# Optimization experiments

Measured on AMD Instinct MI355X. Metric: run time of the kernel, lower is better.

The kernel has to match this reference:

```python
import jax, jax.numpy as jnp
import numpy as np

B, LQ, LK, D = 32, 2048, 2048, 64


def setup_inputs() -> dict:
    key = jax.random.key(0)
    k1, k2, k3, k4 = jax.random.split(key, 4)
    querys = jax.random.normal(k1, (B, LQ, D), dtype=jnp.float32)
    keys = jax.random.normal(k2, (B, LK, D), dtype=jnp.float32)
    values = jax.random.normal(k3, (B, LK, D), dtype=jnp.float32)
    # valid lengths in [1, LK]
    valid_lens = jax.random.randint(k4, (B,), 1, LK + 1, dtype=jnp.int32)
    return {"querys": querys, "keys": keys, "values": values, "valid_lens": valid_lens}


def reference(querys, keys, values, valid_lens):
    d = querys.shape[-1]
    # [B, Lq, Lk] score matrix
    scores = jnp.einsum("bqd,bkd->bqk", querys, keys) / jnp.sqrt(jnp.asarray(d, querys.dtype))
    # masked softmax: key positions >= valid_len get -1e6 (as in d2l masked_softmax)
    key_pos = jnp.arange(scores.shape[-1], dtype=jnp.int32)  # [Lk]
    mask = key_pos[None, None, :] < valid_lens[:, None, None]  # [B, 1, Lk]
    scores = jnp.where(mask, scores, jnp.asarray(-1e6, scores.dtype))
    attn = jax.nn.softmax(scores, axis=-1)
    # dropout p=0.0 -> identity
    return jnp.einsum("bqk,bkd->bqd", attn, values)
```

## Files before the change

### kernel.cpp

```cpp
#include <hip/hip_runtime.h>
#include <hip/hip_bf16.h>
#include <math.h>


#define B_    32
#define LQ_   2048
#define LK_   2048
#define D_    64

typedef __attribute__((ext_vector_type(8)))  short bf16x8;
typedef __attribute__((ext_vector_type(4)))  float f32x4;
typedef __attribute__((ext_vector_type(16))) float f32x16;

static __device__ __forceinline__ unsigned pk_bf16(float a, float b) {
    __hip_bfloat162 h = __float22bfloat162_rn(float2{a, b});
    return *(unsigned*)&h;
}

__global__ __launch_bounds__(128, 2) void fa_mfma3_kernel(
    const float* __restrict__ Q, const float* __restrict__ K,
    const float* __restrict__ V, const int* __restrict__ vlen,
    float* __restrict__ O)
{
    __shared__ __align__(16) short Kl[2][64 * 64];
    __shared__ __align__(16) short Vt[2][64 * 64];

    const int tid  = threadIdx.x;
    const int wave = tid >> 6;
    const int lane = tid & 63;
    const int c31  = lane & 31;
    const int h    = lane >> 5;

    const int b  = blockIdx.y;
    const int q0 = blockIdx.x * 64 + wave * 32;
    const int vl = vlen[b];
    const int nt = (vl + 63) >> 6;

    const float qscale = 0.125f * 1.44269504088896340736f;

    unsigned qfrag[4][4];
#pragma unroll
    for (int ks = 0; ks < 4; ++ks) {
        const float* qp = Q + ((size_t)(b * LQ_ + q0 + c31)) * D_ + ks * 16 + h * 8;
        f32x4 t0 = *(const f32x4*)qp;
        f32x4 t1 = *(const f32x4*)(qp + 4);
#pragma unroll
        for (int jj = 0; jj < 2; ++jj) {
            qfrag[ks][jj]     = pk_bf16(t0[2*jj] * qscale, t0[2*jj+1] * qscale);
            qfrag[ks][jj + 2] = pk_bf16(t1[2*jj] * qscale, t1[2*jj+1] * qscale);
        }
    }

    f32x16 oacc[2];
#pragma unroll
    for (int dt = 0; dt < 2; ++dt)
#pragma unroll
        for (int r = 0; r < 16; ++r) oacc[dt][r] = 0.f;
    float mrun = -INFINITY, lrun = 0.f;

    const int skey = tid >> 1, skh = tid & 1;
    const int vkg = tid >> 4, vdg = tid & 15;

    const float* kgp = K + ((size_t)(b * LK_ + skey)) * D_ + skh * 32;
    const float* vgp = V + ((size_t)(b * LK_ + vkg * 8)) * D_ + vdg * 4;

    f32x4 kr[8], vr[8];
#pragma unroll
    for (int i = 0; i < 8; ++i) kr[i] = *(const f32x4*)(kgp + 4 * i);
#pragma unroll
    for (int i = 0; i < 8; ++i) vr[i] = *(const f32x4*)(vgp + (size_t)i * D_);

    for (int t = 0; t < nt; ++t) {
        const int k0 = t * 64;
        const int buf = t & 1;

        {
            unsigned pk32[16];
#pragma unroll
            for (int m = 0; m < 16; ++m)
                pk32[m] = pk_bf16(kr[m >> 1][2 * (m & 1)], kr[m >> 1][2 * (m & 1) + 1]);
#pragma unroll
            for (int cch = 0; cch < 4; ++cch) {
                const int pos = (skh * 4 + cch) ^ (skey & 7);
                *(bf16x8*)&Kl[buf][skey * 64 + pos * 8] = *(bf16x8*)&pk32[4 * cch];
            }
#pragma unroll
            for (int dr = 0; dr < 4; ++dr) {
                unsigned w[4];
#pragma unroll
                for (int p = 0; p < 4; ++p)
                    w[p] = pk_bf16(vr[2 * p][dr], vr[2 * p + 1][dr]);
                const int dim = vdg * 4 + dr;
                const int pos = vkg ^ (dim & 7);
                *(bf16x8*)&Vt[buf][dim * 64 + pos * 8] = *(bf16x8*)&w[0];
            }
        }
        if (t + 1 < nt) {
            const float* kn = kgp + (size_t)(k0 + 64) * D_;
            const float* vn = vgp + (size_t)(k0 + 64) * D_;
#pragma unroll
            for (int i = 0; i < 8; ++i) kr[i] = *(const f32x4*)(kn + 4 * i);
#pragma unroll
            for (int i = 0; i < 8; ++i) vr[i] = *(const f32x4*)(vn + (size_t)i * D_);
        }
        __syncthreads();

        f32x16 st[2];
#pragma unroll
        for (int s = 0; s < 2; ++s) {
#pragma unroll
            for (int r = 0; r < 16; ++r) st[s][r] = 0.f;
#pragma unroll
            for (int ks = 0; ks < 4; ++ks) {
                const int pos = (ks * 2 + h) ^ (c31 & 7);
                bf16x8 kf = *(const bf16x8*)&Kl[buf][(s * 32 + c31) * 64 + pos * 8];
                st[s] = __builtin_amdgcn_mfma_f32_32x32x16_bf16(
                    kf, *(const bf16x8*)&qfrag[ks][0], st[s], 0, 0, 0);
            }
        }

        if (k0 + 64 > vl) {
#pragma unroll
            for (int s = 0; s < 2; ++s) {
                const int base = k0 + s * 32 + 4 * h;
#pragma unroll
                for (int r = 0; r < 16; ++r) {
                    const int key = base + (r & 3) + 8 * (r >> 2);
                    if (key >= vl) st[s][r] = -1e30f;
                }
            }
        }

        float tm = st[0][0];
#pragma unroll
        for (int s = 0; s < 2; ++s)
#pragma unroll
            for (int r = 0; r < 16; ++r) tm = fmaxf(tm, st[s][r]);
        tm = fmaxf(tm, __shfl_xor(tm, 32));
        const float mnew = fmaxf(mrun, tm);
        const float corr = exp2f(mrun - mnew);
        mrun = mnew;
        float rs = 0.f;
#pragma unroll
        for (int s = 0; s < 2; ++s)
#pragma unroll
            for (int r = 0; r < 16; ++r) {
                const float p = exp2f(st[s][r] - mnew);
                st[s][r] = p;
                rs += p;
            }
        rs += __shfl_xor(rs, 32);
        lrun = lrun * corr + rs;
#pragma unroll
        for (int dt = 0; dt < 2; ++dt)
#pragma unroll
            for (int r = 0; r < 16; ++r) oacc[dt][r] *= corr;

        unsigned pk[2][8];
#pragma unroll
        for (int s = 0; s < 2; ++s)
#pragma unroll
            for (int m = 0; m < 8; ++m)
                pk[s][m] = pk_bf16(st[s][2 * m], st[s][2 * m + 1]);

#pragma unroll
        for (int kq = 0; kq < 4; ++kq) {
            const int s = kq >> 1, A4 = (kq & 1) * 4;
            unsigned p0 = pk[s][A4], p1 = pk[s][A4+1], p2 = pk[s][A4+2], p3 = pk[s][A4+3];
            unsigned xp0 = __shfl_xor((int)p0, 32);
            unsigned xp1 = __shfl_xor((int)p1, 32);
            unsigned xp2 = __shfl_xor((int)p2, 32);
            unsigned xp3 = __shfl_xor((int)p3, 32);
            unsigned pf[4];
            pf[0] = h ? xp2 : p0;
            pf[1] = h ? xp3 : p1;
            pf[2] = h ? p2  : xp0;
            pf[3] = h ? p3  : xp1;
            const bf16x8 pfr = *(const bf16x8*)&pf[0];
#pragma unroll
            for (int dt = 0; dt < 2; ++dt) {
                const int pos = (kq * 2 + h) ^ (c31 & 7);
                bf16x8 vf = *(const bf16x8*)&Vt[buf][(dt * 32 + c31) * 64 + pos * 8];
                oacc[dt] = __builtin_amdgcn_mfma_f32_32x32x16_bf16(vf, pfr, oacc[dt], 0, 0, 0);
            }
        }
    }

    const float inv = 1.f / lrun;
    float* op = O + ((size_t)(b * LQ_ + q0 + c31)) * D_;
#pragma unroll
    for (int dt = 0; dt < 2; ++dt)
#pragma unroll
        for (int g = 0; g < 4; ++g) {
            f32x4 v;
#pragma unroll
            for (int j = 0; j < 4; ++j) v[j] = oacc[dt][4 * g + j] * inv;
            *(f32x4*)(op + dt * 32 + 8 * g + 4 * h) = v;
        }
}

extern "C" void kernel_launch(void* const* d_in, const int* in_sizes, int n_in,
                              void* d_out, int out_size, void* d_ws, size_t ws_size,
                              hipStream_t stream) {
    const float* Q    = (const float*)d_in[0];
    const float* K    = (const float*)d_in[1];
    const float* V    = (const float*)d_in[2];
    const int*   vlen = (const int*)d_in[3];
    float*       O    = (float*)d_out;

    dim3 grid(LQ_ / 64, B_);
    dim3 block(128);
    fa_mfma3_kernel<<<grid, block, 0, stream>>>(Q, K, V, vlen, O);
}
```

Baseline: 172.1 us.

## Split key dimension across chunks with a separate combine kernel

Adds a split-K (flash-decoding style) scheme in which each block handles one key chunk of up to four and writes unnormalized partial outputs plus running max and sum to workspace. A second kernel merges the chunks with log-sum-exp rescaling. The aim is to balance the load across batches with very different valid lengths and to fill the GPU with more blocks. In exchange it adds workspace traffic and an extra launch, and it drops K/V LDS double buffering so more blocks fit per CU. It also changes the V load mapping, uses the native exp2 builtin, and splits the max and sum reductions into parallel chains.

Result: slower. 305.3 us (+77.5%).

```diff
diff --git a/kernel.cpp b/kernel.cpp
--- a/kernel.cpp
+++ b/kernel.cpp
@@ -7,23 +7,31 @@
 #define LQ_   2048
 #define LK_   2048
 #define D_    64
+#define SLOTF (64 * 64 + 128)
 
 typedef __attribute__((ext_vector_type(8)))  short bf16x8;
 typedef __attribute__((ext_vector_type(4)))  float f32x4;
 typedef __attribute__((ext_vector_type(16))) float f32x16;
 
+#if defined(__has_builtin) && __has_builtin(__builtin_amdgcn_exp2f)
+#define EXP2(x) __builtin_amdgcn_exp2f(x)
+#else
+#define EXP2(x) exp2f(x)
+#endif
+
 static __device__ __forceinline__ unsigned pk_bf16(float a, float b) {
     __hip_bfloat162 h = __float22bfloat162_rn(float2{a, b});
     return *(unsigned*)&h;
 }
 
-__global__ __launch_bounds__(128, 2) void fa_mfma3_kernel(
+__global__ __launch_bounds__(128, 4) void fa_stage1(
     const float* __restrict__ Q, const float* __restrict__ K,
     const float* __restrict__ V, const int* __restrict__ vlen,
-    float* __restrict__ O)
+    float* __restrict__ O, float* __restrict__ ws,
+    int nchunks, int chunk_len, int direct)
 {
-    __shared__ __align__(16) short Kl[2][64 * 64];
-    __shared__ __align__(16) short Vt[2][64 * 64];
+    __shared__ __align__(16) short Kl[64 * 64];
+    __shared__ __align__(16) short Vt[64 * 64];
 
     const int tid  = threadIdx.x;
     const int wave = tid >> 6;
@@ -31,10 +39,13 @@
     const int c31  = lane & 31;
     const int h    = lane >> 5;
 
-    const int b  = blockIdx.y;
-    const int q0 = blockIdx.x * 64 + wave * 32;
+    const int qt = blockIdx.x, b = blockIdx.y, cidx = blockIdx.z;
     const int vl = vlen[b];
-    const int nt = (vl + 63) >> 6;
+    const int k_begin = cidx * chunk_len;
+    if (k_begin >= vl) return;
+    const int k_end = min(k_begin + chunk_len, vl);
+    const int nt = (k_end - k_begin + 63) >> 6;
+    const int q0 = qt * 64 + wave * 32;
 
     const float qscale = 0.125f * 1.44269504088896340736f;
 
@@ -59,10 +70,10 @@
     float mrun = -INFINITY, lrun = 0.f;
 
     const int skey = tid >> 1, skh = tid & 1;
-    const int vkg = tid >> 4, vdg = tid & 15;
-
-    const float* kgp = K + ((size_t)(b * LK_ + skey)) * D_ + skh * 32;
-    const float* vgp = V + ((size_t)(b * LK_ + vkg * 8)) * D_ + vdg * 4;
+    const int vkg  = tid & 7,  vdg = tid >> 3;
+
+    const float* kgp = K + ((size_t)(b * LK_ + k_begin + skey)) * D_ + skh * 32;
+    const float* vgp = V + ((size_t)(b * LK_ + k_begin + vkg * 8)) * D_ + vdg * 4;
 
     f32x4 kr[8], vr[8];
 #pragma unroll
@@ -71,8 +82,8 @@
     for (int i = 0; i < 8; ++i) vr[i] = *(const f32x4*)(vgp + (size_t)i * D_);
 
     for (int t = 0; t < nt; ++t) {
-        const int k0 = t * 64;
-        const int buf = t & 1;
+        const int k0 = k_begin + t * 64;
+        if (t) __syncthreads();
 
         {
             unsigned pk32[16];
@@ -82,7 +93,7 @@
 #pragma unroll
             for (int cch = 0; cch < 4; ++cch) {
                 const int pos = (skh * 4 + cch) ^ (skey & 7);
-                *(bf16x8*)&Kl[buf][skey * 64 + pos * 8] = *(bf16x8*)&pk32[4 * cch];
+                *(bf16x8*)&Kl[skey * 64 + pos * 8] = *(bf16x8*)&pk32[4 * cch];
             }
 #pragma unroll
             for (int dr = 0; dr < 4; ++dr) {
@@ -92,12 +103,12 @@
                     w[p] = pk_bf16(vr[2 * p][dr], vr[2 * p + 1][dr]);
                 const int dim = vdg * 4 + dr;
                 const int pos = vkg ^ (dim & 7);
-                *(bf16x8*)&Vt[buf][dim * 64 + pos * 8] = *(bf16x8*)&w[0];
+                *(bf16x8*)&Vt[dim * 64 + pos * 8] = *(bf16x8*)&w[0];
             }
         }
         if (t + 1 < nt) {
-            const float* kn = kgp + (size_t)(k0 + 64) * D_;
-            const float* vn = vgp + (size_t)(k0 + 64) * D_;
+            const float* kn = kgp + (size_t)(t + 1) * 64 * D_;
+            const float* vn = vgp + (size_t)(t + 1) * 64 * D_;
 #pragma unroll
             for (int i = 0; i < 8; ++i) kr[i] = *(const f32x4*)(kn + 4 * i);
 #pragma unroll
@@ -113,7 +124,7 @@
 #pragma unroll
             for (int ks = 0; ks < 4; ++ks) {
                 const int pos = (ks * 2 + h) ^ (c31 & 7);
-                bf16x8 kf = *(const bf16x8*)&Kl[buf][(s * 32 + c31) * 64 + pos * 8];
+                bf16x8 kf = *(const bf16x8*)&Kl[(s * 32 + c31) * 64 + pos * 8];
                 st[s] = __builtin_amdgcn_mfma_f32_32x32x16_bf16(
                     kf, *(const bf16x8*)&qfrag[ks][0], st[s], 0, 0, 0);
             }
@@ -131,24 +142,32 @@
             }
         }
 
-        float tm = st[0][0];
+        float mg[8];
 #pragma unroll
         for (int s = 0; s < 2; ++s)
 #pragma unroll
-            for (int r = 0; r < 16; ++r) tm = fmaxf(tm, st[s][r]);
+            for (int g = 0; g < 4; ++g)
+                mg[s * 4 + g] = fmaxf(fmaxf(st[s][4*g], st[s][4*g+1]),
+                                      fmaxf(st[s][4*g+2], st[s][4*g+3]));
+        float tm = fmaxf(fmaxf(fmaxf(mg[0], mg[1]), fmaxf(mg[2], mg[3])),
+                         fmaxf(fmaxf(mg[4], mg[5]), fmaxf(mg[6], mg[7])));
         tm = fmaxf(tm, __shfl_xor(tm, 32));
         const float mnew = fmaxf(mrun, tm);
-        const float corr = exp2f(mrun - mnew);
+        const float corr = EXP2(mrun - mnew);
         mrun = mnew;
-        float rs = 0.f;
+        float rs0 = 0.f, rs1 = 0.f, rs2 = 0.f, rs3 = 0.f;
 #pragma unroll
         for (int s = 0; s < 2; ++s)
 #pragma unroll
-            for (int r = 0; r < 16; ++r) {
-                const float p = exp2f(st[s][r] - mnew);
-                st[s][r] = p;
-                rs += p;
-            }
+            for (int g = 0; g < 4; ++g) {
+                float p0 = EXP2(st[s][4*g]   - mnew);
+                float p1 = EXP2(st[s][4*g+1] - mnew);
+                float p2 = EXP2(st[s][4*g+2] - mnew);
+                float p3 = EXP2(st[s][4*g+3] - mnew);
+                st[s][4*g] = p0; st[s][4*g+1] = p1; st[s][4*g+2] = p2; st[s][4*g+3] = p3;
+                rs0 += p0; rs1 += p1; rs2 += p2; rs3 += p3;
+            }
+        float rs = (rs0 + rs1) + (rs2 + rs3);
         rs += __shfl_xor(rs, 32);
         lrun = lrun * corr + rs;
 #pragma unroll
@@ -180,23 +199,72 @@
 #pragma unroll
             for (int dt = 0; dt < 2; ++dt) {
                 const int pos = (kq * 2 + h) ^ (c31 & 7);
-                bf16x8 vf = *(const bf16x8*)&Vt[buf][(dt * 32 + c31) * 64 + pos * 8];
+                bf16x8 vf = *(const bf16x8*)&Vt[(dt * 32 + c31) * 64 + pos * 8];
                 oacc[dt] = __builtin_amdgcn_mfma_f32_32x32x16_bf16(vf, pfr, oacc[dt], 0, 0, 0);
             }
         }
     }
 
-    const float inv = 1.f / lrun;
-    float* op = O + ((size_t)(b * LQ_ + q0 + c31)) * D_;
-#pragma unroll
-    for (int dt = 0; dt < 2; ++dt)
-#pragma unroll
-        for (int g = 0; g < 4; ++g) {
-            f32x4 v;
-#pragma unroll
-            for (int j = 0; j < 4; ++j) v[j] = oacc[dt][4 * g + j] * inv;
-            *(f32x4*)(op + dt * 32 + 8 * g + 4 * h) = v;
-        }
+    if (direct) {
+        const float inv = 1.f / lrun;
+        float* op = O + ((size_t)(b * LQ_ + q0 + c31)) * D_;
+#pragma unroll
+        for (int dt = 0; dt < 2; ++dt)
+#pragma unroll
+            for (int g = 0; g < 4; ++g) {
+                f32x4 v;
+#pragma unroll
+                for (int j = 0; j < 4; ++j) v[j] = oacc[dt][4 * g + j] * inv;
+                *(f32x4*)(op + dt * 32 + 8 * g + 4 * h) = v;
+            }
+    } else {
+        float* base = ws + (size_t)((b * 32 + qt) * nchunks + cidx) * SLOTF;
+        float* pp = base + (size_t)(wave * 32 + c31) * D_;
+#pragma unroll
+        for (int dt = 0; dt < 2; ++dt)
+#pragma unroll
+            for (int g = 0; g < 4; ++g) {
+                f32x4 v;
+#pragma unroll
+                for (int j = 0; j < 4; ++j) v[j] = oacc[dt][4 * g + j];
+                *(f32x4*)(pp + dt * 32 + 8 * g + 4 * h) = v;
+            }
+        if (h == 0) {
+            base[64 * 64 + wave * 32 + c31]      = mrun;
+            base[64 * 64 + 64 + wave * 32 + c31] = lrun;
+        }
+    }
+}
+
+__global__ __launch_bounds__(256) void fa_combine(
+    const float* __restrict__ ws, const int* __restrict__ vlen,
+    float* __restrict__ O, int nchunks, int chunk_len)
+{
+    const int idx = blockIdx.x * 256 + threadIdx.x;
+    const int b  = idx >> 15;
+    const int r  = idx & 32767;
+    const int q  = r >> 4;
+    const int dg = r & 15;
+    const int vl = vlen[b];
+    const int nc = min(nchunks, (vl + chunk_len - 1) / chunk_len);
+    const int qt = q >> 6, ql = q & 63;
+    const size_t sbase = (size_t)((b * 32 + qt) * nchunks) * SLOTF;
+
+    float M = -INFINITY;
+    for (int c = 0; c < nc; ++c)
+        M = fmaxf(M, ws[sbase + (size_t)c * SLOTF + 64 * 64 + ql]);
+
+    f32x4 acc = (f32x4){0.f, 0.f, 0.f, 0.f};
+    float L = 0.f;
+    for (int c = 0; c < nc; ++c) {
+        const float* sb = ws + sbase + (size_t)c * SLOTF;
+        const float w = EXP2(sb[64 * 64 + ql] - M);
+        L += sb[64 * 64 + 64 + ql] * w;
+        f32x4 o4 = *(const f32x4*)(sb + (size_t)ql * D_ + dg * 4);
+        acc += o4 * w;
+    }
+    const float inv = 1.f / L;
+    *(f32x4*)(O + (size_t)(b * LQ_ + q) * D_ + dg * 4) = acc * inv;
 }
 
 extern "C" void kernel_launch(void* const* d_in, const int* in_sizes, int n_in,
@@ -207,8 +275,17 @@
     const float* V    = (const float*)d_in[2];
     const int*   vlen = (const int*)d_in[3];
     float*       O    = (float*)d_out;
-
-    dim3 grid(LQ_ / 64, B_);
-    dim3 block(128);
-    fa_mfma3_kernel<<<grid, block, 0, stream>>>(Q, K, V, vlen, O);
-}
+    float*       ws   = (float*)d_ws;
+
+    int S = 4;
+    while (S > 1 && (size_t)B_ * 32 * S * SLOTF * 4 > ws_size) S >>= 1;
+    const int direct = ((size_t)B_ * 32 * S * SLOTF * 4 > ws_size) ? 1 : 0;
+    const int chunk_len = LK_ / S;
+
+    dim3 grid(LQ_ / 64, B_, S);
+    fa_stage1<<<grid, dim3(128), 0, stream>>>(Q, K, V, vlen, O, ws, S, chunk_len, direct);
+    if (!direct) {
+        const int nthreads = B_ * LQ_ * 16;
+        fa_combine<<<dim3(nthreads / 256), dim3(256), 0, stream>>>(ws, vlen, O, S, chunk_len);
+    }
+}
```
